# Kernel optimization log

Hardware: AMD Instinct MI355X
Metric: run time of the kernel (lower is better)

## Reference

```python
import jax, jax.numpy as jnp
import numpy as np

GRID_SIZE = 5
SPLINE_ORDER = 3
GRID_RANGE = (-1.0, 1.0)


def b_splines(x, grid, spline_order=SPLINE_ORDER):
    # x: [B, in], grid: [G] with G = grid_size + 2*spline_order + 1
    x = x[..., None]                      # [B, in, 1]
    g = grid[None, None, :]               # [1, 1, G]
    bases = ((x >= g[..., :-1]) & (x < g[..., 1:])).astype(x.dtype)  # [B, in, G-1]
    for k in range(1, spline_order + 1):
        left = (x - g[..., :-(k + 1)]) / (g[..., k:-1] - g[..., :-(k + 1)]) * bases[..., :-1]
        right = (g[..., k + 1:] - x) / (g[..., k + 1:] - g[..., 1:-k]) * bases[..., 1:]
        bases = left + right
    return bases                          # [B, in, grid_size + spline_order]


def setup_inputs() -> dict:
    key = jax.random.key(0)
    k1, k2, k3, k4 = jax.random.split(key, 4)
    B, IN, OUT = 32768, 256, 256
    n_coef = GRID_SIZE + SPLINE_ORDER  # 8
    h = (GRID_RANGE[1] - GRID_RANGE[0]) / GRID_SIZE
    grid = jnp.arange(-SPLINE_ORDER, GRID_SIZE + SPLINE_ORDER + 1, dtype=jnp.float32) * h + GRID_RANGE[0]  # [12]
    x = jax.random.normal(k1, (B, IN), dtype=jnp.float32)
    base_weight = jax.random.normal(k2, (OUT, IN), dtype=jnp.float32) * np.sqrt(2.0 / IN)
    spline_weight = jax.random.normal(k3, (OUT, IN, n_coef), dtype=jnp.float32) * (0.1 / GRID_SIZE)
    spline_scaler = jax.random.normal(k4, (OUT, IN), dtype=jnp.float32) * np.sqrt(2.0 / IN)
    return {"x": x, "base_weight": base_weight, "spline_weight": spline_weight,
            "spline_scaler": spline_scaler, "grid": grid}


def reference(x, base_weight, spline_weight, spline_scaler, grid):
    B = x.shape[0]
    out_features = base_weight.shape[0]
    # base branch: silu(x) @ base_weight^T
    base_out = jnp.matmul(jax.nn.silu(x), base_weight.T)  # [B, out]
    # spline branch
    bases = b_splines(x, grid)                             # [B, in, n_coef]
    scaled_w = spline_weight * spline_scaler[..., None]    # [out, in, n_coef]
    spline_out = jnp.matmul(bases.reshape(B, -1), scaled_w.reshape(out_features, -1).T)
    return base_out + spline_out
```

## Files before the change

### kernel.cpp

```cpp
#include <hip/hip_runtime.h>
#include <stdint.h>


#define IN_F 256
#define OUT_F 256
#define KDIM 2304
#define BK 64
#define NCHUNK (KDIM / BK)
#define TBINS 512
#define NTAB (11 * TBINS)
#define NTAB_PAD (NTAB + 2)
#define WC_BYTES ((size_t)OUT_F * KDIM * 2)
#define LDS_BYTES (80 * 1024)

#define AS1 __attribute__((address_space(1)))
#define AS3 __attribute__((address_space(3)))

typedef float f32x4 __attribute__((ext_vector_type(4)));
typedef short bf16x8 __attribute__((ext_vector_type(8)));

__device__ __forceinline__ uint32_t f2bf(float f) {
    union { float f; uint32_t u; } c; c.f = f;
    uint32_t u = c.u;
    return (u + 0x7FFFu + ((u >> 16) & 1u)) >> 16;
}

__device__ __forceinline__ float silu_f(float v) {
    return v / (1.0f + __expf(-v));
}

__global__ void build_w(const float* __restrict__ bw, const float* __restrict__ sw,
                        const float* __restrict__ ss, unsigned short* __restrict__ Wc,
                        uint4* __restrict__ tgt) {
    const int o = blockIdx.x;
    const int i = threadIdx.x;
    Wc[o * KDIM + i] = (unsigned short)f2bf(bw[o * IN_F + i]);
    const float scal = ss[o * IN_F + i];
    const float4* swv = reinterpret_cast<const float4*>(sw + (size_t)(o * IN_F + i) * 8);
    float4 s0 = swv[0], s1 = swv[1];
    uint4 wv;
    wv.x = f2bf(s0.x * scal) | (f2bf(s0.y * scal) << 16);
    wv.y = f2bf(s0.z * scal) | (f2bf(s0.w * scal) << 16);
    wv.z = f2bf(s1.x * scal) | (f2bf(s1.y * scal) << 16);
    wv.w = f2bf(s1.z * scal) | (f2bf(s1.w * scal) << 16);
    *reinterpret_cast<uint4*>(Wc + o * KDIM + IN_F + i * 8) = wv;

    if (o == 0) {
        for (int e = i; e < NTAB_PAD; e += IN_F) {
            uint32_t h[4] = {0u, 0u, 0u, 0u};
            if (e >= 1 && e <= NTAB) {
                const int idx = e - 1;
                const int j0 = idx >> 9;
                const float t = ((idx & (TBINS - 1)) + 0.5f) * (1.0f / TBINS);
                const float t2 = t * t, t3 = t2 * t;
                float p[4];
                p[3] = t3 * (1.0f / 6.0f);
                p[2] = -0.5f * t3 + 0.5f * t2 + 0.5f * t + (1.0f / 6.0f);
                p[1] = 0.5f * t3 - t2 + (2.0f / 3.0f);
                const float omt = 1.0f - t;
                p[0] = omt * omt * omt * (1.0f / 6.0f);
#pragma unroll
                for (int m = 0; m < 4; ++m) {
                    int c = j0 - 3 + m;
                    if (c >= 0 && c < 8) h[c >> 1] |= f2bf(p[m]) << ((c & 1) * 16);
                }
            }
            uint4 e4; e4.x = h[0]; e4.y = h[1]; e4.z = h[2]; e4.w = h[3];
            tgt[e] = e4;
        }
    }
}

__launch_bounds__(512, 4)
__global__ void kan_fused(const float* __restrict__ x, const unsigned short* __restrict__ Wc,
                          const uint4* __restrict__ tgt, float* __restrict__ out) {
    extern __shared__ __align__(16) unsigned short smem[];
    unsigned short* const Asb = smem;
    unsigned short* const Bsb = smem + 2 * 64 * 64;

    const int bid = blockIdx.x;
    const int row0 = bid * 64;
    const int tid = threadIdx.x;
    const int lane = tid & 63;
    const int w = tid >> 6;
    const int wm = w >> 2;
    const int wn = w & 3;
    const int l15 = lane & 15;
    const int q = lane >> 4;

    const int sr = lane >> 3;
    const int s  = lane & 7;
    const int g  = s ^ sr;
    const int arow = w * 8 + sr;
    const int brow = w * 32 + sr;

    f32x4 acc[2][4] = {};
    float xrE[8], xrO[8];
    uint4 pkE, pkO;

    auto stage_b = [&](int kc, int buf) {
#pragma unroll
        for (int j = 0; j < 4; ++j) {
            const unsigned short* gp =
                Wc + (size_t)(brow + j * 8) * KDIM + kc * BK + g * 8;
            __builtin_amdgcn_global_load_lds((const AS1 void*)gp,
                (AS3 void*)(Bsb + buf * (256 * 64) + (w * 32 + j * 8) * 64), 16, 0, 0);
        }
    };
    auto load_x = [&](int c, float* xr, uint4& pk) {
        if (c < 4) {
            const float* xp = x + (size_t)(row0 + arow) * IN_F + c * 64 + g * 8;
            float4 a = *reinterpret_cast<const float4*>(xp);
            float4 b = *reinterpret_cast<const float4*>(xp + 4);
            xr[0] = a.x; xr[1] = a.y; xr[2] = a.z; xr[3] = a.w;
            xr[4] = b.x; xr[5] = b.y; xr[6] = b.z; xr[7] = b.w;
        } else {
            const int i0 = (c - 4) * 8 + g;
            float xx = x[(size_t)(row0 + arow) * IN_F + i0];
            float u = __builtin_fmaf(xx, 2.5f, 5.5f);
            int ic = (int)floorf(u * (float)TBINS);
            ic = ic < -1 ? -1 : (ic > NTAB ? NTAB : ic);
            pk = tgt[ic + 1];
        }
    };
    auto write_a = [&](int c, int buf, const float* xr, const uint4& pk) {
        uint4 wv;
        if (c < 4) {
            wv.x = f2bf(silu_f(xr[0])) | (f2bf(silu_f(xr[1])) << 16);
            wv.y = f2bf(silu_f(xr[2])) | (f2bf(silu_f(xr[3])) << 16);
            wv.z = f2bf(silu_f(xr[4])) | (f2bf(silu_f(xr[5])) << 16);
            wv.w = f2bf(silu_f(xr[6])) | (f2bf(silu_f(xr[7])) << 16);
        } else {
            wv = pk;
        }
        *reinterpret_cast<uint4*>(Asb + buf * (64 * 64) + arow * 64 + s * 8) = wv;
    };
    auto mfma_block = [&](int cur) {
        const unsigned short* Ac = Asb + cur * (64 * 64);
        const unsigned short* Bc = Bsb + cur * (256 * 64);
#pragma unroll
        for (int kk = 0; kk < BK; kk += 32) {
            bf16x8 af[2], bfv[4];
            const int g0 = (kk >> 3) + q;
#pragma unroll
            for (int mt = 0; mt < 2; ++mt) {
                int r = wm * 32 + mt * 16 + l15;
                af[mt] = *reinterpret_cast<const bf16x8*>(
                    Ac + r * 64 + ((g0 ^ (r & 7)) << 3));
            }
#pragma unroll
            for (int nt = 0; nt < 4; ++nt) {
                int r = wn * 64 + nt * 16 + l15;
                bfv[nt] = *reinterpret_cast<const bf16x8*>(
                    Bc + r * 64 + ((g0 ^ (r & 7)) << 3));
            }
            __builtin_amdgcn_s_setprio(1);
#pragma unroll
            for (int mt = 0; mt < 2; ++mt)
#pragma unroll
                for (int nt = 0; nt < 4; ++nt)
                    acc[mt][nt] = __builtin_amdgcn_mfma_f32_16x16x32_bf16(
                        af[mt], bfv[nt], acc[mt][nt], 0, 0, 0);
            __builtin_amdgcn_s_setprio(0);
        }
    };

    stage_b(0, 0);
    load_x(0, xrE, pkE);
    write_a(0, 0, xrE, pkE);
    load_x(1, xrO, pkO);
    __syncthreads();

    for (int kc = 0; kc < NCHUNK; kc += 2) {
        {
            if (kc + 1 < NCHUNK) stage_b(kc + 1, 1);
            if (kc + 2 < NCHUNK) load_x(kc + 2, xrE, pkE);
            mfma_block(0);
            if (kc + 1 < NCHUNK) write_a(kc + 1, 1, xrO, pkO);
            __syncthreads();
        }
        {
            if (kc + 2 < NCHUNK) stage_b(kc + 2, 0);
            if (kc + 3 < NCHUNK) load_x(kc + 3, xrO, pkO);
            mfma_block(1);
            if (kc + 2 < NCHUNK) write_a(kc + 2, 0, xrE, pkE);
            __syncthreads();
        }
    }

#pragma unroll
    for (int mt = 0; mt < 2; ++mt) {
        int row = row0 + wm * 32 + mt * 16 + q * 4;
#pragma unroll
        for (int nt = 0; nt < 4; ++nt) {
            int col = wn * 64 + nt * 16 + l15;
#pragma unroll
            for (int r = 0; r < 4; ++r)
                out[(size_t)(row + r) * OUT_F + col] = acc[mt][nt][r];
        }
    }
}

extern "C" void kernel_launch(void* const* d_in, const int* in_sizes, int n_in,
                              void* d_out, int out_size, void* d_ws, size_t ws_size,
                              hipStream_t stream) {
    const float* x  = (const float*)d_in[0];
    const float* bw = (const float*)d_in[1];
    const float* sw = (const float*)d_in[2];
    const float* ss = (const float*)d_in[3];
    unsigned short* Wc = (unsigned short*)d_ws;
    uint4* tgt = (uint4*)((char*)d_ws + WC_BYTES);

    static bool attr_set = false;
    if (!attr_set) {
        (void)hipFuncSetAttribute(reinterpret_cast<const void*>(kan_fused),
                                  hipFuncAttributeMaxDynamicSharedMemorySize,
                                  LDS_BYTES);
        attr_set = true;
    }

    build_w<<<dim3(OUT_F), dim3(IN_F), 0, stream>>>(bw, sw, ss, Wc, tgt);

    const int B_ROWS = in_sizes[0] / IN_F;
    kan_fused<<<dim3(B_ROWS / 64), dim3(512), LDS_BYTES, stream>>>(
        x, Wc, tgt, (float*)d_out);
}
```

Baseline: 145.5 us.

## Load weight fragments directly into registers and double block rows to 128

The weight operand is no longer staged into LDS with async global-to-LDS copies. Each wave now reads its MFMA B fragments straight from global memory (L2-resident) into registers, double-buffered at 32-wide k granularity. The block grows to 1024 threads covering 128 rows, and LDS holds only the double-buffered A tile. The SiLU conversion moves into the load step. This removes LDS traffic and a barrier dependency for B, but the four waves sharing a column slice now fetch the same weights redundantly, and each MFMA step is exposed to global-load latency.

Result: slower. 239.9 us (+64.9%).

```diff
diff --git a/kernel.cpp b/kernel.cpp
--- a/kernel.cpp
+++ b/kernel.cpp
@@ -11,7 +11,6 @@
 #define NTAB (11 * TBINS)
 #define NTAB_PAD (NTAB + 2)
 #define WC_BYTES ((size_t)OUT_F * KDIM * 2)
-#define LDS_BYTES (80 * 1024)
 
 #define AS1 __attribute__((address_space(1)))
 #define AS3 __attribute__((address_space(3)))
@@ -71,15 +70,13 @@
     }
 }
 
-__launch_bounds__(512, 4)
+__launch_bounds__(1024, 4)
 __global__ void kan_fused(const float* __restrict__ x, const unsigned short* __restrict__ Wc,
                           const uint4* __restrict__ tgt, float* __restrict__ out) {
-    extern __shared__ __align__(16) unsigned short smem[];
-    unsigned short* const Asb = smem;
-    unsigned short* const Bsb = smem + 2 * 64 * 64;
+    __shared__ __align__(16) unsigned short As[2][128 * 64];
 
     const int bid = blockIdx.x;
-    const int row0 = bid * 64;
+    const int row0 = bid * 128;
     const int tid = threadIdx.x;
     const int lane = tid & 63;
     const int w = tid >> 6;
@@ -92,28 +89,28 @@
     const int s  = lane & 7;
     const int g  = s ^ sr;
     const int arow = w * 8 + sr;
-    const int brow = w * 32 + sr;
 
     f32x4 acc[2][4] = {};
-    float xrE[8], xrO[8];
     uint4 pkE, pkO;
-
-    auto stage_b = [&](int kc, int buf) {
-#pragma unroll
-        for (int j = 0; j < 4; ++j) {
-            const unsigned short* gp =
-                Wc + (size_t)(brow + j * 8) * KDIM + kc * BK + g * 8;
-            __builtin_amdgcn_global_load_lds((const AS1 void*)gp,
-                (AS3 void*)(Bsb + buf * (256 * 64) + (w * 32 + j * 8) * 64), 16, 0, 0);
-        }
-    };
-    auto load_x = [&](int c, float* xr, uint4& pk) {
+    bf16x8 bA[4], bB[4];
+
+    const unsigned short* wrow = Wc + (size_t)(wn * 64 + l15) * KDIM + q * 8;
+
+    auto load_b = [&](bf16x8* dst, int kc, int kk) {
+#pragma unroll
+        for (int nt = 0; nt < 4; ++nt)
+            dst[nt] = *reinterpret_cast<const bf16x8*>(
+                wrow + (size_t)nt * (16 * KDIM) + kc * BK + kk);
+    };
+    auto load_x = [&](int c, uint4& pk) {
         if (c < 4) {
             const float* xp = x + (size_t)(row0 + arow) * IN_F + c * 64 + g * 8;
             float4 a = *reinterpret_cast<const float4*>(xp);
             float4 b = *reinterpret_cast<const float4*>(xp + 4);
-            xr[0] = a.x; xr[1] = a.y; xr[2] = a.z; xr[3] = a.w;
-            xr[4] = b.x; xr[5] = b.y; xr[6] = b.z; xr[7] = b.w;
+            pk.x = f2bf(silu_f(a.x)) | (f2bf(silu_f(a.y)) << 16);
+            pk.y = f2bf(silu_f(a.z)) | (f2bf(silu_f(a.w)) << 16);
+            pk.z = f2bf(silu_f(b.x)) | (f2bf(silu_f(b.y)) << 16);
+            pk.w = f2bf(silu_f(b.z)) | (f2bf(silu_f(b.w)) << 16);
         } else {
             const int i0 = (c - 4) * 8 + g;
             float xx = x[(size_t)(row0 + arow) * IN_F + i0];
@@ -123,67 +120,51 @@
             pk = tgt[ic + 1];
         }
     };
-    auto write_a = [&](int c, int buf, const float* xr, const uint4& pk) {
-        uint4 wv;
-        if (c < 4) {
-            wv.x = f2bf(silu_f(xr[0])) | (f2bf(silu_f(xr[1])) << 16);
-            wv.y = f2bf(silu_f(xr[2])) | (f2bf(silu_f(xr[3])) << 16);
-            wv.z = f2bf(silu_f(xr[4])) | (f2bf(silu_f(xr[5])) << 16);
-            wv.w = f2bf(silu_f(xr[6])) | (f2bf(silu_f(xr[7])) << 16);
-        } else {
-            wv = pk;
-        }
-        *reinterpret_cast<uint4*>(Asb + buf * (64 * 64) + arow * 64 + s * 8) = wv;
-    };
-    auto mfma_block = [&](int cur) {
-        const unsigned short* Ac = Asb + cur * (64 * 64);
-        const unsigned short* Bc = Bsb + cur * (256 * 64);
-#pragma unroll
-        for (int kk = 0; kk < BK; kk += 32) {
-            bf16x8 af[2], bfv[4];
-            const int g0 = (kk >> 3) + q;
-#pragma unroll
-            for (int mt = 0; mt < 2; ++mt) {
-                int r = wm * 32 + mt * 16 + l15;
-                af[mt] = *reinterpret_cast<const bf16x8*>(
-                    Ac + r * 64 + ((g0 ^ (r & 7)) << 3));
-            }
-#pragma unroll
-            for (int nt = 0; nt < 4; ++nt) {
-                int r = wn * 64 + nt * 16 + l15;
-                bfv[nt] = *reinterpret_cast<const bf16x8*>(
-                    Bc + r * 64 + ((g0 ^ (r & 7)) << 3));
-            }
-            __builtin_amdgcn_s_setprio(1);
-#pragma unroll
-            for (int mt = 0; mt < 2; ++mt)
-#pragma unroll
-                for (int nt = 0; nt < 4; ++nt)
-                    acc[mt][nt] = __builtin_amdgcn_mfma_f32_16x16x32_bf16(
-                        af[mt], bfv[nt], acc[mt][nt], 0, 0, 0);
-            __builtin_amdgcn_s_setprio(0);
-        }
-    };
-
-    stage_b(0, 0);
-    load_x(0, xrE, pkE);
-    write_a(0, 0, xrE, pkE);
-    load_x(1, xrO, pkO);
+    auto write_a = [&](int buf, const uint4& pk) {
+        *reinterpret_cast<uint4*>(&As[buf][arow * 64 + s * 8]) = pk;
+    };
+    auto mfma_kk = [&](int cur, int kk, const bf16x8* bv) {
+        bf16x8 af[2];
+        const int g0 = (kk >> 3) + q;
+#pragma unroll
+        for (int mt = 0; mt < 2; ++mt) {
+            int r = wm * 32 + mt * 16 + l15;
+            af[mt] = *reinterpret_cast<const bf16x8*>(
+                &As[cur][r * 64 + ((g0 ^ (r & 7)) << 3)]);
+        }
+        __builtin_amdgcn_s_setprio(1);
+#pragma unroll
+        for (int mt = 0; mt < 2; ++mt)
+#pragma unroll
+            for (int nt = 0; nt < 4; ++nt)
+                acc[mt][nt] = __builtin_amdgcn_mfma_f32_16x16x32_bf16(
+                    af[mt], bv[nt], acc[mt][nt], 0, 0, 0);
+        __builtin_amdgcn_s_setprio(0);
+    };
+
+    load_x(0, pkE);
+    write_a(0, pkE);
+    load_x(1, pkO);
+    load_b(bA, 0, 0);
     __syncthreads();
 
     for (int kc = 0; kc < NCHUNK; kc += 2) {
         {
-            if (kc + 1 < NCHUNK) stage_b(kc + 1, 1);
-            if (kc + 2 < NCHUNK) load_x(kc + 2, xrE, pkE);
-            mfma_block(0);
-            if (kc + 1 < NCHUNK) write_a(kc + 1, 1, xrO, pkO);
+            load_b(bB, kc, 32);
+            if (kc + 2 < NCHUNK) load_x(kc + 2, pkE);
+            mfma_kk(0, 0, bA);
+            if (kc + 1 < NCHUNK) load_b(bA, kc + 1, 0);
+            mfma_kk(0, 32, bB);
+            if (kc + 1 < NCHUNK) write_a(1, pkO);
             __syncthreads();
         }
         {
-            if (kc + 2 < NCHUNK) stage_b(kc + 2, 0);
-            if (kc + 3 < NCHUNK) load_x(kc + 3, xrO, pkO);
-            mfma_block(1);
-            if (kc + 2 < NCHUNK) write_a(kc + 2, 0, xrE, pkE);
+            load_b(bB, kc + 1, 32);
+            if (kc + 3 < NCHUNK) load_x(kc + 3, pkO);
+            mfma_kk(1, 0, bA);
+            if (kc + 2 < NCHUNK) load_b(bA, kc + 2, 0);
+            mfma_kk(1, 32, bB);
+            if (kc + 2 < NCHUNK) write_a(0, pkE);
             __syncthreads();
         }
     }
@@ -211,17 +192,9 @@
     unsigned short* Wc = (unsigned short*)d_ws;
     uint4* tgt = (uint4*)((char*)d_ws + WC_BYTES);
 
-    static bool attr_set = false;
-    if (!attr_set) {
-        (void)hipFuncSetAttribute(reinterpret_cast<const void*>(kan_fused),
-                                  hipFuncAttributeMaxDynamicSharedMemorySize,
-                                  LDS_BYTES);
-        attr_set = true;
-    }
-
     build_w<<<dim3(OUT_F), dim3(IN_F), 0, stream>>>(bw, sw, ss, Wc, tgt);
 
     const int B_ROWS = in_sizes[0] / IN_F;
-    kan_fused<<<dim3(B_ROWS / 64), dim3(512), LDS_BYTES, stream>>>(
+    kan_fused<<<dim3(B_ROWS / 128), dim3(1024), 0, stream>>>(
         x, Wc, tgt, (float*)d_out);
 }
```

## Build A fragments directly in registers and double the row tile to 128

Applied to the files above, without the earlier changes.

The A operand (silu of x for the base part, table-lookup B-spline bases for the spline part) is no longer staged through LDS. Each wave now computes its MFMA A fragments straight into registers one chunk ahead, and only the weight matrix is staged in LDS. Each block now covers 128 rows instead of 64, so every weight tile in LDS feeds twice as many MFMAs and the LDS writes and reads for A go away. The cost is more registers (16 accumulators plus two prefetch fragment sets) and occupancy bounds cut from 4 to 2 blocks. Each x element may also be loaded and converted redundantly by the waves that share rows (waves with the same wm and different wn).

Result: slower. 231.4 us (+59.1%).

```diff
diff --git a/kernel.cpp b/kernel.cpp
--- a/kernel.cpp
+++ b/kernel.cpp
@@ -11,7 +11,6 @@
 #define NTAB (11 * TBINS)
 #define NTAB_PAD (NTAB + 2)
 #define WC_BYTES ((size_t)OUT_F * KDIM * 2)
-#define LDS_BYTES (80 * 1024)
 
 #define AS1 __attribute__((address_space(1)))
 #define AS3 __attribute__((address_space(3)))
@@ -71,15 +70,13 @@
     }
 }
 
-__launch_bounds__(512, 4)
+__launch_bounds__(512, 2)
 __global__ void kan_fused(const float* __restrict__ x, const unsigned short* __restrict__ Wc,
                           const uint4* __restrict__ tgt, float* __restrict__ out) {
-    extern __shared__ __align__(16) unsigned short smem[];
-    unsigned short* const Asb = smem;
-    unsigned short* const Bsb = smem + 2 * 64 * 64;
+    __shared__ __align__(16) unsigned short Bs[2][256 * 64];
 
     const int bid = blockIdx.x;
-    const int row0 = bid * 64;
+    const int row0 = bid * 128;
     const int tid = threadIdx.x;
     const int lane = tid & 63;
     const int w = tid >> 6;
@@ -91,12 +88,10 @@
     const int sr = lane >> 3;
     const int s  = lane & 7;
     const int g  = s ^ sr;
-    const int arow = w * 8 + sr;
     const int brow = w * 32 + sr;
 
-    f32x4 acc[2][4] = {};
-    float xrE[8], xrO[8];
-    uint4 pkE, pkO;
+    f32x4 acc[4][4] = {};
+    bf16x8 afE[2][4], afO[2][4];
 
     auto stage_b = [&](int kc, int buf) {
 #pragma unroll
@@ -104,93 +99,88 @@
             const unsigned short* gp =
                 Wc + (size_t)(brow + j * 8) * KDIM + kc * BK + g * 8;
             __builtin_amdgcn_global_load_lds((const AS1 void*)gp,
-                (AS3 void*)(Bsb + buf * (256 * 64) + (w * 32 + j * 8) * 64), 16, 0, 0);
+                (AS3 void*)(&Bs[buf][(w * 32 + j * 8) * 64]), 16, 0, 0);
         }
     };
-    auto load_x = [&](int c, float* xr, uint4& pk) {
-        if (c < 4) {
-            const float* xp = x + (size_t)(row0 + arow) * IN_F + c * 64 + g * 8;
-            float4 a = *reinterpret_cast<const float4*>(xp);
-            float4 b = *reinterpret_cast<const float4*>(xp + 4);
-            xr[0] = a.x; xr[1] = a.y; xr[2] = a.z; xr[3] = a.w;
-            xr[4] = b.x; xr[5] = b.y; xr[6] = b.z; xr[7] = b.w;
+
+    auto prefetch = [&](int kc, bf16x8 (&dst)[2][4]) {
+        if (kc < 4) {
+#pragma unroll
+            for (int kkh = 0; kkh < 2; ++kkh)
+#pragma unroll
+                for (int mt = 0; mt < 4; ++mt) {
+                    const int row = row0 + wm * 64 + mt * 16 + l15;
+                    const float* xp = x + (size_t)row * IN_F + kc * 64 + kkh * 32 + q * 8;
+                    float4 a = *reinterpret_cast<const float4*>(xp);
+                    float4 b = *reinterpret_cast<const float4*>(xp + 4);
+                    uint4 wv;
+                    wv.x = f2bf(silu_f(a.x)) | (f2bf(silu_f(a.y)) << 16);
+                    wv.y = f2bf(silu_f(a.z)) | (f2bf(silu_f(a.w)) << 16);
+                    wv.z = f2bf(silu_f(b.x)) | (f2bf(silu_f(b.y)) << 16);
+                    wv.w = f2bf(silu_f(b.z)) | (f2bf(silu_f(b.w)) << 16);
+                    dst[kkh][mt] = *reinterpret_cast<bf16x8*>(&wv);
+                }
         } else {
-            const int i0 = (c - 4) * 8 + g;
-            float xx = x[(size_t)(row0 + arow) * IN_F + i0];
-            float u = __builtin_fmaf(xx, 2.5f, 5.5f);
-            int ic = (int)floorf(u * (float)TBINS);
-            ic = ic < -1 ? -1 : (ic > NTAB ? NTAB : ic);
-            pk = tgt[ic + 1];
+#pragma unroll
+            for (int kkh = 0; kkh < 2; ++kkh)
+#pragma unroll
+                for (int mt = 0; mt < 4; ++mt) {
+                    const int row = row0 + wm * 64 + mt * 16 + l15;
+                    const int feat = kc * 8 + kkh * 4 + q - 32;
+                    float xx = x[(size_t)row * IN_F + feat];
+                    float u = __builtin_fmaf(xx, 2.5f, 5.5f);
+                    int ic = (int)floorf(u * (float)TBINS);
+                    ic = ic < -1 ? -1 : (ic > NTAB ? NTAB : ic);
+                    uint4 t = tgt[ic + 1];
+                    dst[kkh][mt] = *reinterpret_cast<bf16x8*>(&t);
+                }
         }
     };
-    auto write_a = [&](int c, int buf, const float* xr, const uint4& pk) {
-        uint4 wv;
-        if (c < 4) {
-            wv.x = f2bf(silu_f(xr[0])) | (f2bf(silu_f(xr[1])) << 16);
-            wv.y = f2bf(silu_f(xr[2])) | (f2bf(silu_f(xr[3])) << 16);
-            wv.z = f2bf(silu_f(xr[4])) | (f2bf(silu_f(xr[5])) << 16);
-            wv.w = f2bf(silu_f(xr[6])) | (f2bf(silu_f(xr[7])) << 16);
-        } else {
-            wv = pk;
-        }
-        *reinterpret_cast<uint4*>(Asb + buf * (64 * 64) + arow * 64 + s * 8) = wv;
-    };
-    auto mfma_block = [&](int cur) {
-        const unsigned short* Ac = Asb + cur * (64 * 64);
-        const unsigned short* Bc = Bsb + cur * (256 * 64);
-#pragma unroll
-        for (int kk = 0; kk < BK; kk += 32) {
-            bf16x8 af[2], bfv[4];
-            const int g0 = (kk >> 3) + q;
-#pragma unroll
-            for (int mt = 0; mt < 2; ++mt) {
-                int r = wm * 32 + mt * 16 + l15;
-                af[mt] = *reinterpret_cast<const bf16x8*>(
-                    Ac + r * 64 + ((g0 ^ (r & 7)) << 3));
-            }
+
+    auto mfma_chunk = [&](int cur, const bf16x8 (&af)[2][4]) {
+        bf16x8 bfv[2][4];
+#pragma unroll
+        for (int kkh = 0; kkh < 2; ++kkh) {
+            const int g0 = kkh * 4 + q;
 #pragma unroll
             for (int nt = 0; nt < 4; ++nt) {
                 int r = wn * 64 + nt * 16 + l15;
-                bfv[nt] = *reinterpret_cast<const bf16x8*>(
-                    Bc + r * 64 + ((g0 ^ (r & 7)) << 3));
+                bfv[kkh][nt] = *reinterpret_cast<const bf16x8*>(
+                    &Bs[cur][r * 64 + ((g0 ^ (r & 7)) << 3)]);
             }
-            __builtin_amdgcn_s_setprio(1);
-#pragma unroll
-            for (int mt = 0; mt < 2; ++mt)
+        }
+        __builtin_amdgcn_s_setprio(1);
+#pragma unroll
+        for (int kkh = 0; kkh < 2; ++kkh)
+#pragma unroll
+            for (int mt = 0; mt < 4; ++mt)
 #pragma unroll
                 for (int nt = 0; nt < 4; ++nt)
                     acc[mt][nt] = __builtin_amdgcn_mfma_f32_16x16x32_bf16(
-                        af[mt], bfv[nt], acc[mt][nt], 0, 0, 0);
-            __builtin_amdgcn_s_setprio(0);
-        }
+                        af[kkh][mt], bfv[kkh][nt], acc[mt][nt], 0, 0, 0);
+        __builtin_amdgcn_s_setprio(0);
     };
 
     stage_b(0, 0);
-    load_x(0, xrE, pkE);
-    write_a(0, 0, xrE, pkE);
-    load_x(1, xrO, pkO);
+    prefetch(0, afE);
     __syncthreads();
 
     for (int kc = 0; kc < NCHUNK; kc += 2) {
         {
-            if (kc + 1 < NCHUNK) stage_b(kc + 1, 1);
-            if (kc + 2 < NCHUNK) load_x(kc + 2, xrE, pkE);
-            mfma_block(0);
-            if (kc + 1 < NCHUNK) write_a(kc + 1, 1, xrO, pkO);
+            if (kc + 1 < NCHUNK) { stage_b(kc + 1, 1); prefetch(kc + 1, afO); }
+            mfma_chunk(0, afE);
             __syncthreads();
         }
         {
-            if (kc + 2 < NCHUNK) stage_b(kc + 2, 0);
-            if (kc + 3 < NCHUNK) load_x(kc + 3, xrO, pkO);
-            mfma_block(1);
-            if (kc + 2 < NCHUNK) write_a(kc + 2, 0, xrE, pkE);
+            if (kc + 2 < NCHUNK) { stage_b(kc + 2, 0); prefetch(kc + 2, afE); }
+            mfma_chunk(1, afO);
             __syncthreads();
         }
     }
 
 #pragma unroll
-    for (int mt = 0; mt < 2; ++mt) {
-        int row = row0 + wm * 32 + mt * 16 + q * 4;
+    for (int mt = 0; mt < 4; ++mt) {
+        int row = row0 + wm * 64 + mt * 16 + q * 4;
 #pragma unroll
         for (int nt = 0; nt < 4; ++nt) {
             int col = wn * 64 + nt * 16 + l15;
@@ -211,17 +201,9 @@
     unsigned short* Wc = (unsigned short*)d_ws;
     uint4* tgt = (uint4*)((char*)d_ws + WC_BYTES);
 
-    static bool attr_set = false;
-    if (!attr_set) {
-        (void)hipFuncSetAttribute(reinterpret_cast<const void*>(kan_fused),
-                                  hipFuncAttributeMaxDynamicSharedMemorySize,
-                                  LDS_BYTES);
-        attr_set = true;
-    }
-
     build_w<<<dim3(OUT_F), dim3(IN_F), 0, stream>>>(bw, sw, ss, Wc, tgt);
 
     const int B_ROWS = in_sizes[0] / IN_F;
-    kan_fused<<<dim3(B_ROWS / 64), dim3(512), LDS_BYTES, stream>>>(
+    kan_fused<<<dim3(B_ROWS / 128), dim3(512), 0, stream>>>(
         x, Wc, tgt, (float*)d_out);
 }
```
